# Performance work log

Measured on AMD Instinct MI355X. Metric: run time of the kernel, lower is better.

## Reference

```python
import jax, jax.numpy as jnp
import numpy as np

N_NODES = 50000
N_EDGES = 600000
FEAT = 128
N_LAYERS = 4


def setup_inputs() -> dict:
    key = jax.random.key(0)
    ks = jax.random.split(key, 7)
    feats = jax.random.normal(ks[0], (N_NODES, FEAT), dtype=jnp.float32)
    src = jax.random.randint(ks[1], (N_EDGES,), 0, N_NODES)
    dst = jax.random.randint(ks[2], (N_EDGES,), 0, N_NODES)
    s = 1.0 / np.sqrt(FEAT)  # torch Linear default init range
    theta_w = jax.random.uniform(ks[3], (N_LAYERS, FEAT, FEAT), jnp.float32, -s, s)
    theta_b = jax.random.uniform(ks[4], (N_LAYERS, FEAT), jnp.float32, -s, s)
    phi_w = jax.random.uniform(ks[5], (N_LAYERS, FEAT, FEAT), jnp.float32, -s, s)
    phi_b = jax.random.uniform(ks[6], (N_LAYERS, FEAT), jnp.float32, -s, s)
    return {"feats": feats, "src": src, "dst": dst,
            "theta_w": theta_w, "theta_b": theta_b,
            "phi_w": phi_w, "phi_b": phi_b}


def _edgeconv(x, src, dst, tw, tb, pw, pb):
    # EdgeConv (Wang et al. 2018): out_i = max_{(j->i) in E} theta(x_j - x_i) + phi(x_i)
    phi = x @ pw.T + pb                       # [N, F] node-level linear (avoid per-edge recompute)
    diff = x[src] - x[dst]                    # [E, F] gather
    msg = diff @ tw.T + tb + phi[dst]         # [E, F]
    agg = jax.ops.segment_max(msg, dst, num_segments=x.shape[0])  # [N, F]
    # nodes with no incoming edges get -inf from segment_max; zero them (DGL convention)
    return jnp.where(jnp.isneginf(agg), jnp.zeros_like(agg), agg)


def reference(feats, src, dst, theta_w, theta_b, phi_w, phi_b):
    x = feats
    for l in range(N_LAYERS):
        x = _edgeconv(x, src, dst, theta_w[l], theta_b[l], phi_w[l], phi_b[l])
        x = jax.nn.relu(x)
    return x
```

## Files before the change

kernel.cpp:

```cpp
#include <hip/hip_runtime.h>

#define FEAT 128
#define SLABS 4

typedef __attribute__((ext_vector_type(8))) _Float16 f16x8;
typedef __attribute__((ext_vector_type(2))) _Float16 f16x2;
typedef __attribute__((ext_vector_type(4))) float f32x4;

static __device__ __forceinline__ int wave_incl_scan(int v, int lane) {
#pragma unroll
    for (int off = 1; off < 64; off <<= 1) {
        int u = __shfl_up(v, off, 64);
        if (lane >= off) v += u;
    }
    return v;
}


__global__ void prep_kernel(const int* __restrict__ src, const int* __restrict__ dst,
                            int* __restrict__ deg4, int E, int slab_size,
                            const float* __restrict__ tw, const float* __restrict__ pw,
                            const float* __restrict__ tb, const float* __restrict__ pb,
                            _Float16* __restrict__ wt, _Float16* __restrict__ wp,
                            float* __restrict__ bsum, int wn, int nbias,
                            const float* __restrict__ x, _Float16* __restrict__ x16, int xn4,
                            int hb, int wb) {
    int bid = blockIdx.x;
    if (bid < hb) {
        int e = bid * 256 + threadIdx.x;
        if (e < E) {
            int sl = src[e] / slab_size;
            atomicAdd(&deg4[dst[e] * SLABS + sl], 1);
        }
    } else if (bid < hb + wb) {
        int i = (bid - hb) * 256 + threadIdx.x;
        if (i < wn) { wt[i] = (_Float16)tw[i]; wp[i] = (_Float16)pw[i]; }
        if (i < nbias) bsum[i] = tb[i] + pb[i];
    } else {
        int i = (bid - hb - wb) * 256 + threadIdx.x;
        if (i < xn4) {
            float4 v = ((const float4*)x)[i];
            f16x2 a, b;
            a[0] = (_Float16)v.x; a[1] = (_Float16)v.y;
            b[0] = (_Float16)v.z; b[1] = (_Float16)v.w;
            ((f16x2*)x16)[i * 2] = a;
            ((f16x2*)x16)[i * 2 + 1] = b;
        }
    }
}


__global__ __launch_bounds__(1024) void scan1_kernel(const int* __restrict__ deg,
                                                     int* __restrict__ row_ptr,
                                                     int* __restrict__ bsum, int N4) {
    int i = blockIdx.x * 1024 + threadIdx.x;
    int lane = threadIdx.x & 63;
    int w = threadIdx.x >> 6;
    int v = (i < N4) ? deg[i] : 0;
    int inc = wave_incl_scan(v, lane);
    __shared__ int wsum[16];
    if (lane == 63) wsum[w] = inc;
    __syncthreads();
    if (w == 0) {
        int s = (lane < 16) ? wsum[lane] : 0;
        int si = wave_incl_scan(s, lane);
        if (lane < 16) wsum[lane] = si - s;
    }
    __syncthreads();
    int exc = inc - v + wsum[w];
    if (i < N4) row_ptr[i] = exc;
    if (threadIdx.x == 1023) bsum[blockIdx.x] = exc + v;
}

__global__ __launch_bounds__(1024) void scan2_kernel(const int* __restrict__ bsum,
                                                     int* __restrict__ boff,
                                                     int* __restrict__ row_ptr,
                                                     int nb, int N4, int E) {
    int tid = threadIdx.x;
    int lane = tid & 63;
    int w = tid >> 6;
    int v = (tid < nb) ? bsum[tid] : 0;
    int inc = wave_incl_scan(v, lane);
    __shared__ int wsum[16];
    if (lane == 63) wsum[w] = inc;
    __syncthreads();
    if (w == 0) {
        int s = (lane < 16) ? wsum[lane] : 0;
        int si = wave_incl_scan(s, lane);
        if (lane < 16) wsum[lane] = si - s;
    }
    __syncthreads();
    if (tid < nb) boff[tid] = inc - v + wsum[w];
    if (tid == 0) row_ptr[N4] = E;
}

__global__ void scan3_kernel(int* __restrict__ row_ptr, const int* __restrict__ boff, int N4) {
    int i = blockIdx.x * blockDim.x + threadIdx.x;
    if (i < N4) row_ptr[i] += boff[i >> 10];
}


static __device__ __forceinline__ void gemm_body(
        int bx,
        const _Float16* __restrict__ x16,
        const _Float16* __restrict__ wt, const _Float16* __restrict__ wp,
        const float* __restrict__ bias,
        _Float16* __restrict__ t16, _Float16* __restrict__ q16, int M) {
    int lane = threadIdx.x & 63;
    int l16 = lane & 15;
    int quad = lane >> 4;
    int cn0 = (threadIdx.x >> 6) * 32;

    f16x8 bt[2][4], bp[2][4];
    float biasv[2];
#pragma unroll
    for (int ct = 0; ct < 2; ++ct) {
        int col = cn0 + ct * 16 + l16;
        biasv[ct] = bias[col];
#pragma unroll
        for (int kk = 0; kk < 4; ++kk) {
            int k = kk * 32 + quad * 8;
            bt[ct][kk] = *(const f16x8*)(wt + (size_t)col * FEAT + k);
            bp[ct][kk] = *(const f16x8*)(wp + (size_t)col * FEAT + k);
        }
    }

    int rbase0 = bx * 128;
#pragma unroll 1
    for (int rs = 0; rs < 8; ++rs) {
        int rbase = rbase0 + rs * 16;
        int row = rbase + l16;
        int rowc = (row < M) ? row : (M - 1);
        f16x8 a[4];
#pragma unroll
        for (int kk = 0; kk < 4; ++kk)
            a[kk] = *(const f16x8*)(x16 + (size_t)rowc * FEAT + kk * 32 + quad * 8);

        f32x4 accT[2] = {{0.f, 0.f, 0.f, 0.f}, {0.f, 0.f, 0.f, 0.f}};
        f32x4 accP[2] = {{0.f, 0.f, 0.f, 0.f}, {0.f, 0.f, 0.f, 0.f}};
#pragma unroll
        for (int kk = 0; kk < 4; ++kk) {
#pragma unroll
            for (int ct = 0; ct < 2; ++ct) {
                accT[ct] = __builtin_amdgcn_mfma_f32_16x16x32_f16(a[kk], bt[ct][kk], accT[ct], 0, 0, 0);
                accP[ct] = __builtin_amdgcn_mfma_f32_16x16x32_f16(a[kk], bp[ct][kk], accP[ct], 0, 0, 0);
            }
        }
#pragma unroll
        for (int ct = 0; ct < 2; ++ct) {
            int col = cn0 + ct * 16 + l16;
#pragma unroll
            for (int r = 0; r < 4; ++r) {
                int ro = rbase + quad * 4 + r;
                if (ro < M) {
                    t16[(size_t)ro * FEAT + col] = (_Float16)accT[ct][r];
                    q16[(size_t)ro * FEAT + col] =
                        (_Float16)(accP[ct][r] - accT[ct][r] + biasv[ct]);
                }
            }
        }
    }
}

__global__ __launch_bounds__(256) void mfma_gemm_kernel(
        const _Float16* __restrict__ x16,
        const _Float16* __restrict__ wt, const _Float16* __restrict__ wp,
        const float* __restrict__ bias,
        _Float16* __restrict__ t16, _Float16* __restrict__ q16, int M) {
    gemm_body(blockIdx.x, x16, wt, wp, bias, t16, q16, M);
}

__global__ __launch_bounds__(256) void fused0_kernel(
        const _Float16* __restrict__ x16,
        const _Float16* __restrict__ wt, const _Float16* __restrict__ wp,
        const float* __restrict__ bias,
        _Float16* __restrict__ t16, _Float16* __restrict__ q16, int M, int gb,
        const int* __restrict__ src, const int* __restrict__ dst,
        const int* __restrict__ row_ptr4, int* __restrict__ fill4,
        int* __restrict__ esrc, int E, int slab_size) {
    if ((int)blockIdx.x < gb) {
        gemm_body(blockIdx.x, x16, wt, wp, bias, t16, q16, M);
    } else {
        int e = (blockIdx.x - gb) * 256 + threadIdx.x;
        if (e < E) {
            int s = src[e];
            int key = dst[e] * SLABS + s / slab_size;
            int pos = row_ptr4[key] + atomicAdd(&fill4[key], 1);
            esrc[pos] = s;
        }
    }
}


static __device__ __forceinline__ f16x8 vmax8(f16x8 a, f16x8 b) {
#pragma unroll
    for (int i = 0; i < 8; ++i) a[i] = (a[i] > b[i]) ? a[i] : b[i];
    return a;
}

static __device__ __forceinline__ f16x8 shfl_xor8(f16x8 v, int m) {
    union { f16x8 h; int i[4]; } u, r;
    u.h = v;
#pragma unroll
    for (int d = 0; d < 4; ++d) r.i[d] = __shfl_xor(u.i[d], m, 64);
    return r.h;
}

__global__ __launch_bounds__(256) void agg_kernel(
        const _Float16* __restrict__ t16, const _Float16* __restrict__ q16,
        const int* __restrict__ row_ptr4, const int* __restrict__ esrc,
        float* __restrict__ outf, _Float16* __restrict__ ox, int N, int E) {
    int wv = threadIdx.x >> 6;
    int lane = threadIdx.x & 63;
    int node = blockIdx.x * 4 + wv;
    if (node >= N) return;
    (void)E;

    int g = lane >> 4;
    int c = lane & 15;

    int beg = row_ptr4[node * SLABS];
    int end = row_ptr4[node * SLABS + SLABS];
    int cnt = end - beg;

    f16x2 qv = *(const f16x2*)(q16 + (size_t)node * FEAT + c * 8 + g * 2);

    const _Float16 NEGINF = (_Float16)(-65504.0f);
    f16x8 m0, m1;
#pragma unroll
    for (int i = 0; i < 8; ++i) { m0[i] = NEGINF; m1[i] = NEGINF; }

    for (int cb = 0; cb < cnt; cb += 64) {
        int lim = cnt - cb; if (lim > 64) lim = 64;
        int a = beg + cb + (lane < lim ? lane : 0);
        int myidx = esrc[a];
        for (int base = 0; base < lim; base += 8) {
            int e0 = base + g;     if (e0 >= lim) e0 = 0;
            int e1 = base + 4 + g; if (e1 >= lim) e1 = 0;
            int i0 = __shfl(myidx, e0, 64);
            int i1 = __shfl(myidx, e1, 64);
            f16x8 v0 = *(const f16x8*)(t16 + (size_t)i0 * FEAT + c * 8);
            f16x8 v1 = *(const f16x8*)(t16 + (size_t)i1 * FEAT + c * 8);
            m0 = vmax8(m0, v0);
            m1 = vmax8(m1, v1);
        }
    }

    f16x8 mm = vmax8(m0, m1);
    mm = vmax8(mm, shfl_xor8(mm, 16));
    mm = vmax8(mm, shfl_xor8(mm, 32));

    union { f16x8 h; int i[4]; } um; um.h = mm;
    int w01 = (g & 1) ? um.i[1] : um.i[0];
    int w23 = (g & 1) ? um.i[3] : um.i[2];
    int w = (g & 2) ? w23 : w01;
    union { int i; f16x2 h; } uw; uw.i = w;

    float o0 = fmaxf((float)uw.h[0] + (float)qv[0], 0.f);
    float o1 = fmaxf((float)uw.h[1] + (float)qv[1], 0.f);

    if (outf) {
        float2 ov = make_float2(o0, o1);
        *(float2*)(outf + (size_t)node * FEAT + c * 8 + g * 2) = ov;
    }
    if (ox) {
        f16x2 oh; oh[0] = (_Float16)o0; oh[1] = (_Float16)o1;
        *(f16x2*)(ox + (size_t)node * FEAT + c * 8 + g * 2) = oh;
    }
}


extern "C" void kernel_launch(void* const* d_in, const int* in_sizes, int n_in,
                              void* d_out, int out_size, void* d_ws, size_t ws_size,
                              hipStream_t stream) {
    const float* feats   = (const float*)d_in[0];
    const int*   src     = (const int*)d_in[1];
    const int*   dst     = (const int*)d_in[2];
    const float* theta_w = (const float*)d_in[3];
    const float* theta_b = (const float*)d_in[4];
    const float* phi_w   = (const float*)d_in[5];
    const float* phi_b   = (const float*)d_in[6];

    const int N = in_sizes[0] / FEAT;
    const int E = in_sizes[1];
    const int L = in_sizes[3] / (FEAT * FEAT);
    const int N4 = N * SLABS;
    const int slab_size = (N + SLABS - 1) / SLABS;

    char* ws = (char*)d_ws;
    size_t off = 0;
    auto alloc = [&](size_t bytes) -> void* {
        void* ptr = ws + off;
        off = (off + bytes + 255) & ~(size_t)255;
        return ptr;
    };
    _Float16* t16 = (_Float16*)alloc((size_t)N * FEAT * 2);
    _Float16* q16 = (_Float16*)alloc((size_t)N * FEAT * 2);
    _Float16* x16 = (_Float16*)alloc((size_t)N * FEAT * 2);
    _Float16* wt16 = (_Float16*)alloc((size_t)L * FEAT * FEAT * 2);
    _Float16* wp16 = (_Float16*)alloc((size_t)L * FEAT * FEAT * 2);
    float* bsum_b = (float*)alloc((size_t)L * FEAT * sizeof(float));
    int* deg4     = (int*)alloc((size_t)N4 * sizeof(int));
    int* fill4    = (int*)alloc((size_t)N4 * sizeof(int));
    int* row_ptr4 = (int*)alloc((size_t)(N4 + 1) * sizeof(int));
    int* esrc     = (int*)alloc((size_t)E * sizeof(int));
    int* bsum     = (int*)alloc(2048 * sizeof(int));
    int* boff     = (int*)alloc(2048 * sizeof(int));
    (void)ws_size;

    hipMemsetAsync(deg4, 0, (size_t)N4 * sizeof(int), stream);
    hipMemsetAsync(fill4, 0, (size_t)N4 * sizeof(int), stream);

    int eb = (E + 255) / 256;
    int wn = L * FEAT * FEAT;
    int wb = (wn + 255) / 256;
    int xn4 = N * FEAT / 4;
    int xb = (xn4 + 255) / 256;
    prep_kernel<<<eb + wb + xb, 256, 0, stream>>>(
        src, dst, deg4, E, slab_size,
        theta_w, phi_w, theta_b, phi_b, wt16, wp16, bsum_b, wn, L * FEAT,
        feats, x16, xn4, eb, wb);

    int nb = (N4 + 1023) >> 10;
    scan1_kernel<<<nb, 1024, 0, stream>>>(deg4, row_ptr4, bsum, N4);
    scan2_kernel<<<1, 1024, 0, stream>>>(bsum, boff, row_ptr4, nb, N4, E);
    scan3_kernel<<<(N4 + 255) / 256, 256, 0, stream>>>(row_ptr4, boff, N4);

    int gb = (N + 127) / 128;
    int ab = (N + 3) / 4;
    for (int l = 0; l < L; ++l) {
        if (l == 0) {
            fused0_kernel<<<gb + eb, 256, 0, stream>>>(
                x16, wt16, wp16, bsum_b, t16, q16, N, gb,
                src, dst, row_ptr4, fill4, esrc, E, slab_size);
        } else {
            mfma_gemm_kernel<<<gb, 256, 0, stream>>>(
                x16,
                wt16 + (size_t)l * FEAT * FEAT,
                wp16 + (size_t)l * FEAT * FEAT,
                bsum_b + (size_t)l * FEAT,
                t16, q16, N);
        }

        bool last = (l == L - 1);
        agg_kernel<<<ab, 256, 0, stream>>>(
            t16, q16,
            row_ptr4, esrc,
            last ? (float*)d_out : nullptr,
            last ? nullptr : x16,
            N, E);
    }
}
```

Baseline: 317.9 us.

## Fuse all layers into one persistent cooperative kernel with grid syncs

Replaces the per-layer sequence of GEMM and aggregation launches with a single cooperative persistent kernel. It fills the CSR edge list, then for each layer runs the GEMM tiles and node aggregations in grid-stride loops, separated by grid.sync(). The aim is to remove kernel launch gaps and tail effects across the eight or so launches. In exchange the grid is capped at occupancy-limited residency, grid-wide barriers add their own cost, and the edge scatter no longer overlaps with the layer-0 GEMM. The old multi-launch path is kept as a fallback if the cooperative launch fails.

```diff
diff --git a/kernel.cpp b/kernel.cpp
--- a/kernel.cpp
+++ b/kernel.cpp
@@ -1,4 +1,7 @@
 #include <hip/hip_runtime.h>
+#include <hip/hip_cooperative_groups.h>
+
+namespace cg = cooperative_groups;
 
 #define FEAT 128
 #define SLABS 4
@@ -101,7 +104,7 @@
 
 
 static __device__ __forceinline__ void gemm_body(
-        int bx,
+        int bx, int nslab,
         const _Float16* __restrict__ x16,
         const _Float16* __restrict__ wt, const _Float16* __restrict__ wp,
         const float* __restrict__ bias,
@@ -125,9 +128,9 @@
         }
     }
 
-    int rbase0 = bx * 128;
+    int rbase0 = bx * (nslab * 16);
 #pragma unroll 1
-    for (int rs = 0; rs < 8; ++rs) {
+    for (int rs = 0; rs < nslab; ++rs) {
         int rbase = rbase0 + rs * 16;
         int row = rbase + l16;
         int rowc = (row < M) ? row : (M - 1);
@@ -162,35 +165,6 @@
     }
 }
 
-__global__ __launch_bounds__(256) void mfma_gemm_kernel(
-        const _Float16* __restrict__ x16,
-        const _Float16* __restrict__ wt, const _Float16* __restrict__ wp,
-        const float* __restrict__ bias,
-        _Float16* __restrict__ t16, _Float16* __restrict__ q16, int M) {
-    gemm_body(blockIdx.x, x16, wt, wp, bias, t16, q16, M);
-}
-
-__global__ __launch_bounds__(256) void fused0_kernel(
-        const _Float16* __restrict__ x16,
-        const _Float16* __restrict__ wt, const _Float16* __restrict__ wp,
-        const float* __restrict__ bias,
-        _Float16* __restrict__ t16, _Float16* __restrict__ q16, int M, int gb,
-        const int* __restrict__ src, const int* __restrict__ dst,
-        const int* __restrict__ row_ptr4, int* __restrict__ fill4,
-        int* __restrict__ esrc, int E, int slab_size) {
-    if ((int)blockIdx.x < gb) {
-        gemm_body(blockIdx.x, x16, wt, wp, bias, t16, q16, M);
-    } else {
-        int e = (blockIdx.x - gb) * 256 + threadIdx.x;
-        if (e < E) {
-            int s = src[e];
-            int key = dst[e] * SLABS + s / slab_size;
-            int pos = row_ptr4[key] + atomicAdd(&fill4[key], 1);
-            esrc[pos] = s;
-        }
-    }
-}
-
 
 static __device__ __forceinline__ f16x8 vmax8(f16x8 a, f16x8 b) {
 #pragma unroll
@@ -206,19 +180,12 @@
     return r.h;
 }
 
-__global__ __launch_bounds__(256) void agg_kernel(
+static __device__ __forceinline__ void agg_node(
+        int node,
         const _Float16* __restrict__ t16, const _Float16* __restrict__ q16,
         const int* __restrict__ row_ptr4, const int* __restrict__ esrc,
-        float* __restrict__ outf, _Float16* __restrict__ ox, int N, int E) {
-    int wv = threadIdx.x >> 6;
-    int lane = threadIdx.x & 63;
-    int node = blockIdx.x * 4 + wv;
-    if (node >= N) return;
-    (void)E;
-
-    int g = lane >> 4;
-    int c = lane & 15;
-
+        float* __restrict__ outf, _Float16* __restrict__ ox,
+        int lane, int g, int c) {
     int beg = row_ptr4[node * SLABS];
     int end = row_ptr4[node * SLABS + SLABS];
     int cnt = end - beg;
@@ -267,6 +234,85 @@
         f16x2 oh; oh[0] = (_Float16)o0; oh[1] = (_Float16)o1;
         *(f16x2*)(ox + (size_t)node * FEAT + c * 8 + g * 2) = oh;
     }
+}
+
+
+__global__ __launch_bounds__(256) void layers_kernel(
+        _Float16* x16, const _Float16* wt16, const _Float16* wp16,
+        const float* bsum_b, _Float16* t16, _Float16* q16,
+        const int* row_ptr4, int* fill4, int* esrc,
+        const int* __restrict__ src, const int* __restrict__ dst,
+        float* outf, int N, int E, int L, int slab_size, int T64) {
+    cg::grid_group grid = cg::this_grid();
+    const int G = gridDim.x;
+    int lane = threadIdx.x & 63;
+    int g = lane >> 4;
+    int c = lane & 15;
+    int wid0 = blockIdx.x * 4 + (threadIdx.x >> 6);
+    int wstride = G * 4;
+
+    for (int e = blockIdx.x * 256 + threadIdx.x; e < E; e += G * 256) {
+        int s = src[e];
+        int key = dst[e] * SLABS + s / slab_size;
+        int pos = row_ptr4[key] + atomicAdd(&fill4[key], 1);
+        esrc[pos] = s;
+    }
+
+    for (int l = 0; l < L; ++l) {
+        const _Float16* wt = wt16 + (size_t)l * FEAT * FEAT;
+        const _Float16* wp = wp16 + (size_t)l * FEAT * FEAT;
+        const float* bias = bsum_b + (size_t)l * FEAT;
+        for (int bx = blockIdx.x; bx < T64; bx += G)
+            gemm_body(bx, 4, x16, wt, wp, bias, t16, q16, N);
+        grid.sync();
+
+        bool last = (l == L - 1);
+        float* of = last ? outf : nullptr;
+        _Float16* oxp = last ? nullptr : x16;
+        for (int node = wid0; node < N; node += wstride)
+            agg_node(node, t16, q16, row_ptr4, esrc, of, oxp, lane, g, c);
+        if (!last) grid.sync();
+    }
+}
+
+
+__global__ __launch_bounds__(256) void mfma_gemm_kernel(
+        const _Float16* __restrict__ x16,
+        const _Float16* __restrict__ wt, const _Float16* __restrict__ wp,
+        const float* __restrict__ bias,
+        _Float16* __restrict__ t16, _Float16* __restrict__ q16, int M) {
+    gemm_body(blockIdx.x, 8, x16, wt, wp, bias, t16, q16, M);
+}
+
+__global__ __launch_bounds__(256) void fused0_kernel(
+        const _Float16* __restrict__ x16,
+        const _Float16* __restrict__ wt, const _Float16* __restrict__ wp,
+        const float* __restrict__ bias,
+        _Float16* __restrict__ t16, _Float16* __restrict__ q16, int M, int gb,
+        const int* __restrict__ src, const int* __restrict__ dst,
+        const int* __restrict__ row_ptr4, int* __restrict__ fill4,
+        int* __restrict__ esrc, int E, int slab_size) {
+    if ((int)blockIdx.x < gb) {
+        gemm_body(blockIdx.x, 8, x16, wt, wp, bias, t16, q16, M);
+    } else {
+        int e = (blockIdx.x - gb) * 256 + threadIdx.x;
+        if (e < E) {
+            int s = src[e];
+            int key = dst[e] * SLABS + s / slab_size;
+            int pos = row_ptr4[key] + atomicAdd(&fill4[key], 1);
+            esrc[pos] = s;
+        }
+    }
+}
+
+__global__ __launch_bounds__(256) void agg_kernel(
+        const _Float16* __restrict__ t16, const _Float16* __restrict__ q16,
+        const int* __restrict__ row_ptr4, const int* __restrict__ esrc,
+        float* __restrict__ outf, _Float16* __restrict__ ox, int N) {
+    int node = blockIdx.x * 4 + (threadIdx.x >> 6);
+    if (node >= N) return;
+    int lane = threadIdx.x & 63;
+    agg_node(node, t16, q16, row_ptr4, esrc, outf, ox, lane, lane >> 4, lane & 15);
 }
 
 
@@ -326,28 +372,65 @@
     scan2_kernel<<<1, 1024, 0, stream>>>(bsum, boff, row_ptr4, nb, N4, E);
     scan3_kernel<<<(N4 + 255) / 256, 256, 0, stream>>>(row_ptr4, boff, N4);
 
-    int gb = (N + 127) / 128;
-    int ab = (N + 3) / 4;
-    for (int l = 0; l < L; ++l) {
-        if (l == 0) {
-            fused0_kernel<<<gb + eb, 256, 0, stream>>>(
-                x16, wt16, wp16, bsum_b, t16, q16, N, gb,
-                src, dst, row_ptr4, fill4, esrc, E, slab_size);
-        } else {
-            mfma_gemm_kernel<<<gb, 256, 0, stream>>>(
-                x16,
-                wt16 + (size_t)l * FEAT * FEAT,
-                wp16 + (size_t)l * FEAT * FEAT,
-                bsum_b + (size_t)l * FEAT,
-                t16, q16, N);
-        }
-
-        bool last = (l == L - 1);
-        agg_kernel<<<ab, 256, 0, stream>>>(
-            t16, q16,
-            row_ptr4, esrc,
-            last ? (float*)d_out : nullptr,
-            last ? nullptr : x16,
-            N, E);
-    }
-}
+    static int s_G = -1;
+    if (s_G < 0) {
+        int nblk = 0, cus = 0, dev = 0;
+        hipGetDevice(&dev);
+        hipDeviceGetAttribute(&cus, hipDeviceAttributeMultiprocessorCount, dev);
+        if (hipOccupancyMaxActiveBlocksPerMultiprocessor(&nblk, layers_kernel, 256, 0)
+                != hipSuccess || nblk < 1 || cus < 1)
+            s_G = 0;
+        else
+            s_G = nblk * cus;
+    }
+
+    int T64 = (N + 63) / 64;
+    bool coop_ok = false;
+    if (s_G > 0) {
+        _Float16* x16a = x16;
+        const _Float16* wt16a = wt16;
+        const _Float16* wp16a = wp16;
+        const float* bsa = bsum_b;
+        _Float16* t16a = t16;
+        _Float16* q16a = q16;
+        const int* rpa = row_ptr4;
+        int* fla = fill4;
+        int* esa = esrc;
+        const int* srca = src;
+        const int* dsta = dst;
+        float* outa = (float*)d_out;
+        int Na = N, Ea = E, La = L, ssa = slab_size, Ta = T64;
+        void* args[] = {&x16a, &wt16a, &wp16a, &bsa, &t16a, &q16a,
+                        &rpa, &fla, &esa, &srca, &dsta, &outa,
+                        &Na, &Ea, &La, &ssa, &Ta};
+        coop_ok = hipLaunchCooperativeKernel((const void*)layers_kernel,
+                                             dim3(s_G), dim3(256), args, 0, stream)
+                  == hipSuccess;
+        if (!coop_ok) s_G = 0;
+    }
+
+    if (!coop_ok) {
+        int gb = (N + 127) / 128;
+        int ab = (N + 3) / 4;
+        for (int l = 0; l < L; ++l) {
+            if (l == 0) {
+                fused0_kernel<<<gb + eb, 256, 0, stream>>>(
+                    x16, wt16, wp16, bsum_b, t16, q16, N, gb,
+                    src, dst, row_ptr4, fill4, esrc, E, slab_size);
+            } else {
+                mfma_gemm_kernel<<<gb, 256, 0, stream>>>(
+                    x16,
+                    wt16 + (size_t)l * FEAT * FEAT,
+                    wp16 + (size_t)l * FEAT * FEAT,
+                    bsum_b + (size_t)l * FEAT,
+                    t16, q16, N);
+            }
+            bool last = (l == L - 1);
+            agg_kernel<<<ab, 256, 0, stream>>>(
+                t16, q16, row_ptr4, esrc,
+                last ? (float*)d_out : nullptr,
+                last ? nullptr : x16,
+                N);
+        }
+    }
+}
```

Result: slower. 854.7 us (+168.8%).
